# Kernel tuning notes

Hardware: AMD Instinct MI355X
Metric: run time of the kernel (lower is better)

Reference implementation:

```python
import jax, jax.numpy as jnp
import numpy as np

B, T, F = 64, 1024, 4
INF = jnp.float32(1e30)


def _dtw_cost(p, q):
    """Accumulated DTW cost matrix. p: [T1,2], q: [T2,2]. Returns C: [T1,T2].

    Recurrence C[i,j] = D[i,j] + min(C[i-1,j], C[i,j-1], C[i-1,j-1]).
    The within-row dependency c_j = d_j + min(a_j, c_{j-1}) (with
    a_j = min(C[i-1,j], C[i-1,j-1])) is a min-plus scan, solved in closed
    form: c_j = S_j + cummin_k<=j (a_k - S_{k-1}), S = cumsum(d).
    """
    # pairwise Euclidean distance (dtw.dtw2d uses 2D Euclidean)
    D = jnp.sqrt(jnp.sum((p[:, None, :] - q[None, :, :]) ** 2, axis=-1))  # [T1,T2]

    c0 = jnp.cumsum(D[0])  # first row: only left moves allowed

    def row(prev, d):
        shifted = jnp.concatenate([jnp.full((1,), INF, prev.dtype), prev[:-1]])
        a = jnp.minimum(prev, shifted)          # min(C[i-1,j], C[i-1,j-1])
        S = jnp.cumsum(d)
        Sprev = jnp.concatenate([jnp.zeros((1,), d.dtype), S[:-1]])
        m = jax.lax.associative_scan(jnp.minimum, a - Sprev)
        c = S + m
        return c, c

    _, rest = jax.lax.scan(row, c0, D[1:])
    return jnp.concatenate([c0[None, :], rest], axis=0)


def _dtw_path(C):
    """Backtrace alignment path from C. Returns (a, b, valid) each [T1+T2-1]."""
    T1, T2 = C.shape
    L = T1 + T2 - 1

    def step(carry, _):
        i, j, done = carry
        at0 = (i == 0) & (j == 0)
        cd = jnp.where((i > 0) & (j > 0), C[i - 1, j - 1], INF)
        cu = jnp.where(i > 0, C[i - 1, j], INF)
        cl = jnp.where(j > 0, C[i, j - 1], INF)
        k = jnp.argmin(jnp.stack([cd, cu, cl]))  # diag preferred on ties
        di = jnp.where(k == 2, 0, 1)
        dj = jnp.where(k == 1, 0, 1)
        ni = jnp.where(at0, 0, i - di)
        nj = jnp.where(at0, 0, j - dj)
        return (ni, nj, done | at0), (i, j, jnp.logical_not(done))

    init = (jnp.int32(T1 - 1), jnp.int32(T2 - 1), jnp.bool_(False))
    _, (a, b, valid) = jax.lax.scan(step, init, None, length=L)
    return a, b, valid


def _single_loss(pred, targ, subcoef):
    # DTW alignment computed on (x, y) basis, detached (torch runs it in numpy)
    p = jax.lax.stop_gradient(pred[:, :2])
    q = jax.lax.stop_gradient(targ[:, :2])
    C = _dtw_cost(p, q)
    a, b, valid = _dtw_path(C)
    # gather aligned points on loss_indices = [0, 1], L1 loss weighted by subcoef
    pg = pred[a, :2]  # [L, 2]
    tg = targ[b, :2]
    w = valid[:, None].astype(pred.dtype)
    return jnp.sum(jnp.abs(pg - tg) * subcoef[None, :] * w)


def setup_inputs() -> dict:
    key = jax.random.key(0)
    k1, k2 = jax.random.split(key)
    preds = jax.random.normal(k1, (B, T, F), dtype=jnp.float32)
    targs = jax.random.normal(k2, (B, T, F), dtype=jnp.float32)
    subcoef = jnp.ones((2,), dtype=jnp.float32)
    return {"preds": preds, "targs": targs, "subcoef": subcoef}


def reference(preds, targs, subcoef):
    losses = jax.vmap(lambda p, t: _single_loss(p, t, subcoef))(preds, targs)
    return jnp.sum(losses)
```

## Files before the change

kernel.cpp:

```cpp
#include <hip/hip_runtime.h>

#define TT   1024
#define NW   34
#define NPH  (NW + 21)
#define FINF 1e30f

template<bool A> struct BoolC { static constexpr bool value = A; };


__device__ __forceinline__ float dpp_shr1_old(float oldv, float x) {
    return __int_as_float(__builtin_amdgcn_update_dpp(
        __float_as_int(oldv), __float_as_int(x), 0x138, 0xF, 0xF, false));
}

__global__ __launch_bounds__(512) void dtw_forward(
    const float* __restrict__ preds,
    const float* __restrict__ targs,
    uint2* __restrict__ dirs)
{
    __shared__ float2 qsh[TT];
    __shared__ float  mbox[7][TT];

    const int tid  = threadIdx.x;
    const int w    = tid >> 6;
    const int lane = tid & 63;
    const int b    = blockIdx.x;

    for (int k = tid; k < TT; k += 512) {
        float4 t4 = ((const float4*)targs)[(size_t)b * TT + k];
        qsh[k] = make_float2(t4.x, t4.y);
    }
    for (int k = tid; k < 7 * TT; k += 512) ((float*)mbox)[k] = FINF;

    float px0, py0, px1, py1;
    {
        const int row0 = w * 128 + 2 * lane;
        float4 pv = ((const float4*)preds)[(size_t)b * TT + row0];
        px0 = pv.x; py0 = pv.y;
        float4 pw = ((const float4*)preds)[(size_t)b * TT + row0 + 1];
        px1 = pw.x; py1 = pw.y;
    }
    __syncthreads();

    const float* src = (w > 0) ? mbox[w - 1] : nullptr;
    float*       dst = (w < 7) ? mbox[w]     : nullptr;

    float cur0 = FINF, cur1 = FINF, uprev = FINF, ucur = FINF;
    unsigned au0 = 0, ad0 = 0, au1 = 0, ad1 = 0;
    unsigned pau0 = 0, pad0 = 0, pau1 = 0, pad1 = 0;
    int pT = -1;

    const int bi  = 2 * w + (lane >> 5);
    const int rr0 = 2 * (lane & 31);
    const bool is63 = (lane == 63);

    for (int G = 0; G < NPH; ++G) {
        if (pT >= 0) {
            const size_t base = (size_t)((b * 16 + bi) * NW + pT) * 64 + rr0;
            *(uint4*)&dirs[base] =
                make_uint4(__builtin_bitreverse32(pau0), __builtin_bitreverse32(pad0),
                           __builtin_bitreverse32(pau1), __builtin_bitreverse32(pad1));
            pT = -1;
        }
        const int T = G - 3 * w;
        if ((unsigned)T < (unsigned)NW) {
            float bnd[33];
#pragma unroll
            for (int k = 0; k < 33; ++k) bnd[k] = FINF;
            if (w > 0) {
#pragma unroll
                for (int k = 0; k < 33; ++k) {
                    const int c = 32 * T + k;
                    if (c < TT) bnd[k] = src[c];
                }
            }
            if (T == 0) ucur = bnd[0];
            float qx[32], qy[32];
#pragma unroll
            for (int k = 0; k < 32; ++k) {
                float2 v = qsh[(32 * T + k - lane) & (TT - 1)];
                qx[k] = v.x; qy[k] = v.y;
            }
            float bq[32];
            auto body = [&](auto actc) {
                constexpr bool ACT = decltype(actc)::value;
#pragma unroll
                for (int k2 = 0; k2 < 32; ++k2) {
                    const int s = 32 * T + k2;
                    const float dx0 = px0 - qx[k2], dy0 = py0 - qy[k2];
                    const float d0 = __builtin_amdgcn_sqrtf(dx0 * dx0 + dy0 * dy0);
                    const float dx1 = px1 - qx[k2], dy1 = py1 - qy[k2];
                    const float d1 = __builtin_amdgcn_sqrtf(dx1 * dx1 + dy1 * dy1);

                    const float u = ucur;
                    float ba0 = fminf(fminf(u, cur0), uprev);
                    const unsigned bd0 = (uprev == ba0) ? 1u : 0u;
                    const unsigned bu0 = ((u <= cur0) ? 1u : 0u) | bd0;
                    if constexpr (ACT) ba0 = (ba0 > 9e29f) ? 0.0f : ba0;
                    const float v0 = d0 + ba0;
                    const float ba1 = fminf(fminf(v0, cur1), cur0);
                    const unsigned bd1 = (cur0 == ba1) ? 1u : 0u;
                    const unsigned bu1 = ((v0 <= cur1) ? 1u : 0u) | bd1;
                    const float v1 = d1 + ba1;

                    au0 = au0 + au0 + bu0;  ad0 = ad0 + ad0 + bd0;
                    au1 = au1 + au1 + bu1;  ad1 = ad1 + ad1 + bd1;

                    if constexpr (ACT) {
                        const bool act = (lane <= s);
                        cur0 = act ? v0 : cur0;
                        cur1 = act ? v1 : cur1;
                    } else {
                        cur0 = v0; cur1 = v1;
                    }
                    uprev = u;
                    bq[k2] = cur1;
                    ucur = dpp_shr1_old(bnd[k2 + 1], cur1);
                }
            };
            if (T < 2) body(BoolC<true>{}); else body(BoolC<false>{});

            if (is63 && w < 7) {
#pragma unroll
                for (int k2 = 0; k2 < 32; ++k2) {
                    const int c = 32 * T + k2 - 63;
                    if ((unsigned)c < 1024u) dst[c] = bq[k2];
                }
            }
            pau0 = au0; pad0 = ad0; pau1 = au1; pad1 = ad1; pT = T;
            au0 = ad0 = au1 = ad1 = 0u;
        }
        __syncthreads();
    }
    if (pT >= 0) {
        const size_t base = (size_t)((b * 16 + bi) * NW + pT) * 64 + rr0;
        *(uint4*)&dirs[base] =
            make_uint4(__builtin_bitreverse32(pau0), __builtin_bitreverse32(pad0),
                       __builtin_bitreverse32(pau1), __builtin_bitreverse32(pad1));
    }
}

__global__ __launch_bounds__(1024) void dtw_exits(
    const uint2* __restrict__ dirs,
    unsigned short* __restrict__ exitc)
{
    __shared__ uint2 raw[NW * 64];
    __shared__ unsigned nebit[64][32];
    __shared__ unsigned dgbit[64][32];
    __shared__ short prevnz[64][32];

    const int tid = threadIdx.x;
    const int b = blockIdx.x >> 4, bi = blockIdx.x & 15;

    for (int i = tid; i < NW * 64; i += 1024)
        raw[i] = dirs[(size_t)(b * 16 + bi) * (NW * 64) + i];
    __syncthreads();
    for (int i = tid; i < 64 * 32; i += 1024) {
        const int rr = i >> 5, u = i & 31;
        const int o  = ((bi & 1) << 5) + (rr >> 1);
        const int T0 = u + (o >> 5), sh = o & 31;
        uint2 A  = raw[T0 * 64 + rr];
        uint2 Bv = raw[(T0 + 1) * 64 + rr];
        nebit[rr][u] = sh ? ((A.x >> sh) | (Bv.x << (32 - sh))) : A.x;
        dgbit[rr][u] = sh ? ((A.y >> sh) | (Bv.y << (32 - sh))) : A.y;
    }
    __syncthreads();
    if (tid < 64) {
        int p = -1;
        for (int u = 0; u < 32; ++u) {
            if (nebit[tid][u] != 0u) p = u;
            prevnz[tid][u] = (short)p;
        }
    }
    __syncthreads();

    int j = tid;
    for (int rr = 63; rr >= 0; --rr) {
        if (bi == 0 && rr == 0) { j = 0; break; }
        const int u = j >> 5, m = j & 31;
        const unsigned wv = nebit[rr][u] << (31 - m);
        int j2;
        if (wv != 0u) j2 = (u << 5) + m - __builtin_clz(wv);
        else {
            const int u2 = (u > 0) ? (int)prevnz[rr][u - 1] : -1;
            j2 = (u2 < 0) ? 0 : ((u2 << 5) + 31 - __builtin_clz(nebit[rr][u2]));
        }
        const int diag = (int)((dgbit[rr][j2 >> 5] >> (j2 & 31)) & 1u);
        j = j2 - diag;
        if (j < 0) j = 0;
    }
    exitc[((size_t)(b * 16 + bi) << 10) + tid] = (unsigned short)j;
}

__global__ __launch_bounds__(64) void dtw_loss(
    const float* __restrict__ preds,
    const float* __restrict__ targs,
    const float* __restrict__ subcoef,
    const uint2* __restrict__ dirs,
    const unsigned short* __restrict__ exitc,
    float* __restrict__ out)
{
    __shared__ uint2 raw[NW * 64];
    __shared__ unsigned nebit[64][32];
    __shared__ unsigned dgbit[64][32];
    __shared__ short prevnz[64][32];
    __shared__ float2 qsh[TT];
    __shared__ float2 psh[64];
    __shared__ unsigned recs[160];

    const int lane = threadIdx.x;
    const int b = blockIdx.x >> 4, bi = blockIdx.x & 15;

    for (int i = lane; i < NW * 64; i += 64)
        raw[i] = dirs[(size_t)(b * 16 + bi) * (NW * 64) + i];
    for (int k = lane; k < TT; k += 64) {
        float4 t4 = ((const float4*)targs)[(size_t)b * TT + k];
        qsh[k] = make_float2(t4.x, t4.y);
    }
    {
        float4 p4 = ((const float4*)preds)[(size_t)b * TT + bi * 64 + lane];
        psh[lane] = make_float2(p4.x, p4.y);
    }
    __syncthreads();
    for (int i = lane; i < 64 * 32; i += 64) {
        const int rr = i >> 5, u = i & 31;
        const int o  = ((bi & 1) << 5) + (rr >> 1);
        const int T0 = u + (o >> 5), sh = o & 31;
        uint2 A  = raw[T0 * 64 + rr];
        uint2 Bv = raw[(T0 + 1) * 64 + rr];
        nebit[rr][u] = sh ? ((A.x >> sh) | (Bv.x << (32 - sh))) : A.x;
        dgbit[rr][u] = sh ? ((A.y >> sh) | (Bv.y << (32 - sh))) : A.y;
    }
    __syncthreads();
    {
        int p = -1;
        for (int u = 0; u < 32; ++u) {
            if (nebit[lane][u] != 0u) p = u;
            prevnz[lane][u] = (short)p;
        }
    }

    int j = TT - 1;
    for (int k = 15; k > bi; --k)
        j = exitc[((size_t)(b * 16 + k) << 10) + j];
    __syncthreads();

    int nrec = 0;
    for (int rr = 63; rr >= 0; --rr) {
        int j2;
        if (bi == 0 && rr == 0) j2 = 0;
        else {
            const int u = j >> 5, m = j & 31;
            const unsigned wv = nebit[rr][u] << (31 - m);
            if (wv != 0u) j2 = (u << 5) + m - __builtin_clz(wv);
            else {
                const int u2 = (u > 0) ? (int)prevnz[rr][u - 1] : -1;
                j2 = (u2 < 0) ? 0 : ((u2 << 5) + 31 - __builtin_clz(nebit[rr][u2]));
            }
        }
        int c = j;
        for (;;) {
            int cl = (c - 31 > j2) ? (c - 31) : j2;
            if (lane == 0)
                recs[nrec] = ((unsigned)rr << 20) | ((unsigned)cl << 10) | (unsigned)c;
            ++nrec;
            if (cl == j2) break;
            c = cl - 1;
        }
        if (bi == 0 && rr == 0) j = 0;
        else {
            const int diag = (int)((dgbit[rr][j2 >> 5] >> (j2 & 31)) & 1u);
            j = j2 - diag;
            if (j < 0) j = 0;
        }
    }
    __syncthreads();

    const float sc0 = subcoef[0], sc1 = subcoef[1];
    float acc = 0.0f;
    for (int k = lane; k < nrec; k += 64) {
        unsigned rec = recs[k];
        int rr = (int)(rec >> 20), cl = (int)((rec >> 10) & 1023u), ch = (int)(rec & 1023u);
        float2 p = psh[rr];
        for (int c = cl; c <= ch; ++c) {
            float2 q = qsh[c];
            acc += fabsf(p.x - q.x) * sc0 + fabsf(p.y - q.y) * sc1;
        }
    }
    for (int o = 32; o; o >>= 1) acc += __shfl_down(acc, o);
    if (lane == 0) atomicAdd(out, acc);
}

extern "C" void kernel_launch(void* const* d_in, const int* in_sizes, int n_in,
                              void* d_out, int out_size, void* d_ws, size_t ws_size,
                              hipStream_t stream)
{
    const float* preds   = (const float*)d_in[0];
    const float* targs   = (const float*)d_in[1];
    const float* subcoef = (const float*)d_in[2];
    float* out = (float*)d_out;

    const int B = in_sizes[0] / (TT * 4);

    const size_t dirsBytes = (size_t)B * 16 * NW * 64 * sizeof(uint2);
    uint2* dirs = (uint2*)d_ws;
    unsigned short* exitc = (unsigned short*)((char*)d_ws + dirsBytes);

    hipMemsetAsync(out, 0, sizeof(float), stream);
    dtw_forward<<<dim3(B), dim3(512), 0, stream>>>(preds, targs, dirs);
    dtw_exits<<<dim3(B * 16), dim3(1024), 0, stream>>>(dirs, exitc);
    dtw_loss<<<dim3(B * 16), dim3(64), 0, stream>>>(preds, targs, subcoef, dirs, exitc, out);
}
```

Baseline: 402.9 us.

## Compute a 2x2 cell block per lane to halve wavefront diagonal steps

```diff
diff --git a/kernel.cpp b/kernel.cpp
--- a/kernel.cpp
+++ b/kernel.cpp
@@ -1,8 +1,9 @@
 #include <hip/hip_runtime.h>
 
 #define TT   1024
-#define NW   34
-#define NPH  (NW + 21)
+#define NR   36
+#define NWP  18
+#define NPH  (NWP + 21)
 #define FINF 1e30f
 
 template<bool A> struct BoolC { static constexpr bool value = A; };
@@ -13,12 +14,12 @@
         __float_as_int(oldv), __float_as_int(x), 0x138, 0xF, 0xF, false));
 }
 
-__global__ __launch_bounds__(512) void dtw_forward(
+__global__ __launch_bounds__(512, 2) void dtw_forward(
     const float* __restrict__ preds,
     const float* __restrict__ targs,
     uint2* __restrict__ dirs)
 {
-    __shared__ float2 qsh[TT];
+    __shared__ float2 qsh[2][512];
     __shared__ float  mbox[7][TT];
 
     const int tid  = threadIdx.x;
@@ -28,7 +29,7 @@
 
     for (int k = tid; k < TT; k += 512) {
         float4 t4 = ((const float4*)targs)[(size_t)b * TT + k];
-        qsh[k] = make_float2(t4.x, t4.y);
+        qsh[k & 1][k >> 1] = make_float2(t4.x, t4.y);
     }
     for (int k = tid; k < 7 * TT; k += 512) ((float*)mbox)[k] = FINF;
 
@@ -37,106 +38,139 @@
         const int row0 = w * 128 + 2 * lane;
         float4 pv = ((const float4*)preds)[(size_t)b * TT + row0];
         px0 = pv.x; py0 = pv.y;
-        float4 pw = ((const float4*)preds)[(size_t)b * TT + row0 + 1];
-        px1 = pw.x; py1 = pw.y;
+        float4 pw2 = ((const float4*)preds)[(size_t)b * TT + row0 + 1];
+        px1 = pw2.x; py1 = pw2.y;
     }
     __syncthreads();
 
     const float* src = (w > 0) ? mbox[w - 1] : nullptr;
     float*       dst = (w < 7) ? mbox[w]     : nullptr;
 
-    float cur0 = FINF, cur1 = FINF, uprev = FINF, ucur = FINF;
-    unsigned au0 = 0, ad0 = 0, au1 = 0, ad1 = 0;
-    unsigned pau0 = 0, pad0 = 0, pau1 = 0, pad1 = 0;
-    int pT = -1;
+    float cur01 = FINF, cur11 = FINF;
+    float uA = FINF, uB = FINF, uBp = FINF;
+    unsigned pA0 = 0, pA1 = 0, pA2 = 0, pA3 = 0;
+    unsigned pB0 = 0, pB1 = 0, pB2 = 0, pB3 = 0;
+    int pP = -1;
 
     const int bi  = 2 * w + (lane >> 5);
     const int rr0 = 2 * (lane & 31);
     const bool is63 = (lane == 63);
 
+    auto runHalf = [&](int T, unsigned& o0, unsigned& o1, unsigned& o2,
+                       unsigned& o3, auto actc) {
+        constexpr bool ACT = decltype(actc)::value;
+        float bnd[34];
+#pragma unroll
+        for (int i = 0; i < 34; ++i) bnd[i] = FINF;
+        if (w > 0) {
+#pragma unroll
+            for (int i = 0; i < 34; ++i) {
+                const int c = 32 * T + i;
+                if (c < TT) bnd[i] = src[c];
+            }
+        }
+        if (T == 0) { uA = bnd[0]; uB = bnd[1]; }
+        float2 qa[16], qb[16];
+#pragma unroll
+        for (int k = 0; k < 16; ++k) {
+            const int m = (16 * T + k - lane) & 511;
+            qa[k] = qsh[0][m];
+            qb[k] = qsh[1][m];
+        }
+        float2 bq[16];
+        unsigned au0 = 0, ad0 = 0, au1 = 0, ad1 = 0;
+#pragma unroll
+        for (int k = 0; k < 16; ++k) {
+            const float dxa0 = px0 - qa[k].x, dya0 = py0 - qa[k].y;
+            const float d00 = __builtin_amdgcn_sqrtf(dxa0 * dxa0 + dya0 * dya0);
+            const float dxb0 = px0 - qb[k].x, dyb0 = py0 - qb[k].y;
+            const float d01 = __builtin_amdgcn_sqrtf(dxb0 * dxb0 + dyb0 * dyb0);
+            const float dxa1 = px1 - qa[k].x, dya1 = py1 - qa[k].y;
+            const float d10 = __builtin_amdgcn_sqrtf(dxa1 * dxa1 + dya1 * dya1);
+            const float dxb1 = px1 - qb[k].x, dyb1 = py1 - qb[k].y;
+            const float d11 = __builtin_amdgcn_sqrtf(dxb1 * dxb1 + dyb1 * dyb1);
+
+            float ba00 = fminf(fminf(uA, cur01), uBp);
+            const unsigned bd00 = (uBp == ba00) ? 1u : 0u;
+            const unsigned bu00 = ((uA <= cur01) ? 1u : 0u) | bd00;
+            if constexpr (ACT) ba00 = (ba00 > 9e29f) ? 0.0f : ba00;
+            const float v00 = d00 + ba00;
+            const float ba01 = fminf(fminf(uB, v00), uA);
+            const unsigned bd01 = (uA == ba01) ? 1u : 0u;
+            const unsigned bu01 = ((uB <= v00) ? 1u : 0u) | bd01;
+            const float v01 = d01 + ba01;
+            const float ba10 = fminf(fminf(v00, cur11), cur01);
+            const unsigned bd10 = (cur01 == ba10) ? 1u : 0u;
+            const unsigned bu10 = ((v00 <= cur11) ? 1u : 0u) | bd10;
+            const float v10 = d10 + ba10;
+            const float ba11 = fminf(fminf(v01, v10), v00);
+            const unsigned bd11 = (v00 == ba11) ? 1u : 0u;
+            const unsigned bu11 = ((v01 <= v10) ? 1u : 0u) | bd11;
+            const float v11 = d11 + ba11;
+
+            au0 = (au0 << 2) | (bu00 << 1) | bu01;
+            ad0 = (ad0 << 2) | (bd00 << 1) | bd01;
+            au1 = (au1 << 2) | (bu10 << 1) | bu11;
+            ad1 = (ad1 << 2) | (bd10 << 1) | bd11;
+
+            float sv10, sv11;
+            if constexpr (ACT) {
+                const bool act = (lane <= 16 * T + k);
+                cur01 = act ? v01 : cur01;
+                cur11 = act ? v11 : cur11;
+                sv10 = act ? v10 : FINF;
+                sv11 = act ? v11 : FINF;
+            } else {
+                cur01 = v01; cur11 = v11;
+                sv10 = v10;  sv11 = v11;
+            }
+            bq[k] = make_float2(sv10, sv11);
+            uBp = uB;
+            uA = dpp_shr1_old(bnd[2 * k + 2], sv10);
+            uB = dpp_shr1_old(bnd[2 * k + 3], sv11);
+        }
+        if (is63 && w < 7) {
+#pragma unroll
+            for (int k = 0; k < 16; ++k) {
+                const int c = 32 * T + 2 * k - 126;
+                if ((unsigned)c < 1024u) *(float2*)&dst[c] = bq[k];
+            }
+        }
+        o0 = au0; o1 = ad0; o2 = au1; o3 = ad1;
+    };
+
     for (int G = 0; G < NPH; ++G) {
-        if (pT >= 0) {
-            const size_t base = (size_t)((b * 16 + bi) * NW + pT) * 64 + rr0;
-            *(uint4*)&dirs[base] =
-                make_uint4(__builtin_bitreverse32(pau0), __builtin_bitreverse32(pad0),
-                           __builtin_bitreverse32(pau1), __builtin_bitreverse32(pad1));
-            pT = -1;
-        }
-        const int T = G - 3 * w;
-        if ((unsigned)T < (unsigned)NW) {
-            float bnd[33];
-#pragma unroll
-            for (int k = 0; k < 33; ++k) bnd[k] = FINF;
-            if (w > 0) {
-#pragma unroll
-                for (int k = 0; k < 33; ++k) {
-                    const int c = 32 * T + k;
-                    if (c < TT) bnd[k] = src[c];
-                }
-            }
-            if (T == 0) ucur = bnd[0];
-            float qx[32], qy[32];
-#pragma unroll
-            for (int k = 0; k < 32; ++k) {
-                float2 v = qsh[(32 * T + k - lane) & (TT - 1)];
-                qx[k] = v.x; qy[k] = v.y;
-            }
-            float bq[32];
-            auto body = [&](auto actc) {
-                constexpr bool ACT = decltype(actc)::value;
-#pragma unroll
-                for (int k2 = 0; k2 < 32; ++k2) {
-                    const int s = 32 * T + k2;
-                    const float dx0 = px0 - qx[k2], dy0 = py0 - qy[k2];
-                    const float d0 = __builtin_amdgcn_sqrtf(dx0 * dx0 + dy0 * dy0);
-                    const float dx1 = px1 - qx[k2], dy1 = py1 - qy[k2];
-                    const float d1 = __builtin_amdgcn_sqrtf(dx1 * dx1 + dy1 * dy1);
-
-                    const float u = ucur;
-                    float ba0 = fminf(fminf(u, cur0), uprev);
-                    const unsigned bd0 = (uprev == ba0) ? 1u : 0u;
-                    const unsigned bu0 = ((u <= cur0) ? 1u : 0u) | bd0;
-                    if constexpr (ACT) ba0 = (ba0 > 9e29f) ? 0.0f : ba0;
-                    const float v0 = d0 + ba0;
-                    const float ba1 = fminf(fminf(v0, cur1), cur0);
-                    const unsigned bd1 = (cur0 == ba1) ? 1u : 0u;
-                    const unsigned bu1 = ((v0 <= cur1) ? 1u : 0u) | bd1;
-                    const float v1 = d1 + ba1;
-
-                    au0 = au0 + au0 + bu0;  ad0 = ad0 + ad0 + bd0;
-                    au1 = au1 + au1 + bu1;  ad1 = ad1 + ad1 + bd1;
-
-                    if constexpr (ACT) {
-                        const bool act = (lane <= s);
-                        cur0 = act ? v0 : cur0;
-                        cur1 = act ? v1 : cur1;
-                    } else {
-                        cur0 = v0; cur1 = v1;
-                    }
-                    uprev = u;
-                    bq[k2] = cur1;
-                    ucur = dpp_shr1_old(bnd[k2 + 1], cur1);
-                }
-            };
-            if (T < 2) body(BoolC<true>{}); else body(BoolC<false>{});
-
-            if (is63 && w < 7) {
-#pragma unroll
-                for (int k2 = 0; k2 < 32; ++k2) {
-                    const int c = 32 * T + k2 - 63;
-                    if ((unsigned)c < 1024u) dst[c] = bq[k2];
-                }
-            }
-            pau0 = au0; pad0 = ad0; pau1 = au1; pad1 = ad1; pT = T;
-            au0 = ad0 = au1 = ad1 = 0u;
+        if (pP >= 0) {
+            const size_t base = (size_t)((b * 16 + bi) * NR + 2 * pP) * 64 + rr0;
+            *(uint4*)&dirs[base] = make_uint4(
+                __builtin_bitreverse32(pA0), __builtin_bitreverse32(pA1),
+                __builtin_bitreverse32(pA2), __builtin_bitreverse32(pA3));
+            *(uint4*)&dirs[base + 64] = make_uint4(
+                __builtin_bitreverse32(pB0), __builtin_bitreverse32(pB1),
+                __builtin_bitreverse32(pB2), __builtin_bitreverse32(pB3));
+            pP = -1;
+        }
+        const int P = G - 3 * w;
+        if ((unsigned)P < (unsigned)NWP) {
+            if (P < 2) {
+                runHalf(2 * P,     pA0, pA1, pA2, pA3, BoolC<true>{});
+                runHalf(2 * P + 1, pB0, pB1, pB2, pB3, BoolC<true>{});
+            } else {
+                runHalf(2 * P,     pA0, pA1, pA2, pA3, BoolC<false>{});
+                runHalf(2 * P + 1, pB0, pB1, pB2, pB3, BoolC<false>{});
+            }
+            pP = P;
         }
         __syncthreads();
     }
-    if (pT >= 0) {
-        const size_t base = (size_t)((b * 16 + bi) * NW + pT) * 64 + rr0;
-        *(uint4*)&dirs[base] =
-            make_uint4(__builtin_bitreverse32(pau0), __builtin_bitreverse32(pad0),
-                       __builtin_bitreverse32(pau1), __builtin_bitreverse32(pad1));
+    if (pP >= 0) {
+        const size_t base = (size_t)((b * 16 + bi) * NR + 2 * pP) * 64 + rr0;
+        *(uint4*)&dirs[base] = make_uint4(
+            __builtin_bitreverse32(pA0), __builtin_bitreverse32(pA1),
+            __builtin_bitreverse32(pA2), __builtin_bitreverse32(pA3));
+        *(uint4*)&dirs[base + 64] = make_uint4(
+            __builtin_bitreverse32(pB0), __builtin_bitreverse32(pB1),
+            __builtin_bitreverse32(pB2), __builtin_bitreverse32(pB3));
     }
 }
 
@@ -144,7 +178,7 @@
     const uint2* __restrict__ dirs,
     unsigned short* __restrict__ exitc)
 {
-    __shared__ uint2 raw[NW * 64];
+    __shared__ uint2 raw[NR * 64];
     __shared__ unsigned nebit[64][32];
     __shared__ unsigned dgbit[64][32];
     __shared__ short prevnz[64][32];
@@ -152,12 +186,12 @@
     const int tid = threadIdx.x;
     const int b = blockIdx.x >> 4, bi = blockIdx.x & 15;
 
-    for (int i = tid; i < NW * 64; i += 1024)
-        raw[i] = dirs[(size_t)(b * 16 + bi) * (NW * 64) + i];
+    for (int i = tid; i < NR * 64; i += 1024)
+        raw[i] = dirs[(size_t)(b * 16 + bi) * (NR * 64) + i];
     __syncthreads();
     for (int i = tid; i < 64 * 32; i += 1024) {
         const int rr = i >> 5, u = i & 31;
-        const int o  = ((bi & 1) << 5) + (rr >> 1);
+        const int o  = (((bi & 1) << 5) + (rr >> 1)) << 1;
         const int T0 = u + (o >> 5), sh = o & 31;
         uint2 A  = raw[T0 * 64 + rr];
         uint2 Bv = raw[(T0 + 1) * 64 + rr];
@@ -200,7 +234,7 @@
     const unsigned short* __restrict__ exitc,
     float* __restrict__ out)
 {
-    __shared__ uint2 raw[NW * 64];
+    __shared__ uint2 raw[NR * 64];
     __shared__ unsigned nebit[64][32];
     __shared__ unsigned dgbit[64][32];
     __shared__ short prevnz[64][32];
@@ -211,8 +245,8 @@
     const int lane = threadIdx.x;
     const int b = blockIdx.x >> 4, bi = blockIdx.x & 15;
 
-    for (int i = lane; i < NW * 64; i += 64)
-        raw[i] = dirs[(size_t)(b * 16 + bi) * (NW * 64) + i];
+    for (int i = lane; i < NR * 64; i += 64)
+        raw[i] = dirs[(size_t)(b * 16 + bi) * (NR * 64) + i];
     for (int k = lane; k < TT; k += 64) {
         float4 t4 = ((const float4*)targs)[(size_t)b * TT + k];
         qsh[k] = make_float2(t4.x, t4.y);
@@ -224,7 +258,7 @@
     __syncthreads();
     for (int i = lane; i < 64 * 32; i += 64) {
         const int rr = i >> 5, u = i & 31;
-        const int o  = ((bi & 1) << 5) + (rr >> 1);
+        const int o  = (((bi & 1) << 5) + (rr >> 1)) << 1;
         const int T0 = u + (o >> 5), sh = o & 31;
         uint2 A  = raw[T0 * 64 + rr];
         uint2 Bv = raw[(T0 + 1) * 64 + rr];
@@ -302,7 +336,7 @@
 
     const int B = in_sizes[0] / (TT * 4);
 
-    const size_t dirsBytes = (size_t)B * 16 * NW * 64 * sizeof(uint2);
+    const size_t dirsBytes = (size_t)B * 16 * NR * 64 * sizeof(uint2);
     uint2* dirs = (uint2*)d_ws;
     unsigned short* exitc = (unsigned short*)((char*)d_ws + dirsBytes);
 
```

Result: slower. 478.3 us (+18.7%).
